# Kernel tuning notes

Hardware: AMD Instinct MI355X
Metric: run time of the kernel (lower is better)

The kernel has to match this reference:

```python
import jax, jax.numpy as jnp
import numpy as np

B, F, T, C, G = 2, 2048, 750, 20, 3
K = int(T * 0.125)  # top-k for score_pre


def _conv1d(x, w, b=None, pad=0):
    # x: (N, Cin, L), w: (Cout, Cin, k)
    out = jax.lax.conv_general_dilated(x, w, (1,), [(pad, pad)],
                                       dimension_numbers=('NCH', 'OIH', 'NCH'))
    return out if b is None else out + b[None, :, None]


def _base(x, w1, b1, w2, b2):
    # BaseModule: two k=3 convs with LeakyReLU(0.01); dropout = identity (eval)
    h = jax.nn.leaky_relu(_conv1d(x, w1, b1, pad=1))
    h = jax.nn.leaky_relu(_conv1d(h, w2, b2, pad=1))
    return h


def _post_cls(feat_agg, w1, b1, w2, b2, wc, batch, g):
    # feat_agg: (batch*C, F, g) -> BaseModule -> grouped 1x1 classifier -> mean over g
    h = _base(feat_agg, w1, b1, w2, b2)            # (batch*C, 2048, g)
    h = h.reshape(batch, C, 2048, g)
    score = jnp.einsum('bckg,ck->bcg', h, wc[:, :, 0])  # grouped conv1d, groups=C
    return score.mean(axis=2)                       # (batch, C)


def setup_inputs():
    key = jax.random.key(0)
    ks = jax.random.split(key, 8)
    s = 0.02
    x = jax.random.normal(ks[0], (B, F, T), jnp.float32)
    w1 = jax.random.normal(ks[1], (2048, F, 3), jnp.float32) * s
    b1 = jnp.zeros((2048,), jnp.float32)
    w2 = jax.random.normal(ks[2], (2048, 2048, 3), jnp.float32) * s
    b2 = jnp.zeros((2048,), jnp.float32)
    wc = jax.random.normal(ks[3], (C, 2048, 1), jnp.float32) * s   # classifier, no bias
    watt = jax.random.normal(ks[4], (C, C, 1), jnp.float32) * s    # attention 1x1 conv
    batt = jnp.zeros((C,), jnp.float32)
    cls_label = (jax.random.uniform(ks[5], (B, C)) < 0.15).astype(jnp.int32)
    cls_label = cls_label.at[:, 0].set(1)  # guarantee >=1 gt class per video
    return {'x': x, 'w1': w1, 'b1': b1, 'w2': w2, 'b2': b2, 'wc': wc,
            'watt': watt, 'batt': batt, 'cls_label': cls_label,
            'groups': G, 'is_train': 1}


def reference(x, w1, b1, w2, b2, wc, watt, batt, cls_label, groups, is_train):
    g = groups
    Tg = T // g
    seq_cas = _conv1d(_base(x, w1, b1, w2, b2), wc)           # (B, C, T)
    score_pre = jax.lax.top_k(seq_cas, K)[0].mean(axis=2)     # (B, C)
    wa = jax.nn.sigmoid(_conv1d(seq_cas, watt, batt))         # (B, C, T) attention weights

    # _agg_feature: strided slice t = j*g + i  <=>  reshape T -> (Tg, g), group idx last
    xg = x.reshape(B, F, Tg, g)
    wag = wa.reshape(B, C, Tg, g)
    feat_agg = jnp.einsum('bcjg,bfjg->bcfg', wag, xg).reshape(B * C, F, g)
    score_post = _post_cls(feat_agg, w1, b1, w2, b2, wc, B, g)  # (B, C)

    if is_train:
        # background stream, vectorized over (batch, suppressed class c) with masking
        wbg = (1.0 - wa).reshape(B, C, Tg, g)
        # tiny intermediate (B,C,C,Tg,g), then contract with features
        ww = jnp.einsum('bajg,bcjg->bcajg', wag, wbg)
        agg = jnp.einsum('bcajg,bfjg->bcafg', ww, xg).reshape(B * C * C, F, g)
        sc = _post_cls(agg, w1, b1, w2, b2, wc, B * C, g).reshape(B, C, C)  # [b, suppressed c, class a]
        m = cls_label.astype(score_post.dtype)                 # (B, C) multi-hot
        ngt = jnp.maximum(m.sum(axis=1, keepdims=True), 1.0)
        collect = jnp.einsum('bc,bca->ba', m, sc) / ngt        # mean over gt classes
        diag = jnp.diagonal(sc, axis1=1, axis2=2)              # sc[b, j, j]
        collect = jnp.where(m > 0, diag, collect)              # overwrite gt entries
        score_agg = jax.nn.softmax(jnp.concatenate([score_post, collect], axis=1), axis=1)
        return (score_pre, score_post, score_agg)
    else:
        return (jax.nn.softmax(score_pre, axis=1), seq_cas)
```

## Files before the change

kernel.cpp:

```cpp
#include <hip/hip_runtime.h>
#include <math.h>

namespace {
constexpr int kF = 2048;
constexpr int kT = 750;
constexpr int kC = 20;
constexpr int kTop = 93;
}

typedef __bf16 bf16x8 __attribute__((ext_vector_type(8)));
typedef float f32x4 __attribute__((ext_vector_type(4)));

__device__ __forceinline__ ushort f2bf(float f) {
  uint u = __builtin_bit_cast(uint, f);
  uint r = u + 0x7FFFu + ((u >> 16) & 1u);
  return (ushort)(r >> 16);
}
__device__ __forceinline__ float bf2f(ushort u) {
  return __builtin_bit_cast(float, ((uint)u) << 16);
}
__device__ __forceinline__ float leaky(float v) { return v > 0.f ? v : 0.01f * v; }

__device__ __forceinline__ void gload_lds16(const ushort* g, ushort* l) {
  __builtin_amdgcn_global_load_lds(
      (const __attribute__((address_space(1))) void*)g,
      (__attribute__((address_space(3))) void*)l, 16, 0, 0);
}

__global__ void build_list_kernel(const int* __restrict__ lbl,
                                  int4* __restrict__ meta, int* __restrict__ cnt) {
  if (threadIdx.x != 0) return;
  int n = 0;
  for (int b = 0; b < 2; ++b) {
    cnt[4 + b] = n;
    for (int c = 0; c < kC; ++c) { meta[n] = make_int4(b, c, c, 1); ++n; }
    for (int c = 0; c < kC; ++c)
      for (int a = 0; a < kC; ++a)
        if (lbl[b * kC + c] > 0 || c == a) { meta[n] = make_int4(b, c, a, 0); ++n; }
    cnt[6 + b] = (n - cnt[4 + b]);
  }
  cnt[0] = n;
  cnt[1] = n * 3;
  cnt[2] = 1500;
  cnt[3] = 0;
}

__global__ __launch_bounds__(256) void convert_w_kernel(
    const float* __restrict__ w1, const float* __restrict__ w2,
    ushort* __restrict__ Wt1, ushort* __restrict__ Wt2,
    ushort* __restrict__ zpage) {
  const int co = blockIdx.x;
  const float* w = (blockIdx.y == 0) ? w1 : w2;
  ushort* Wt = (blockIdx.y == 0) ? Wt1 : Wt2;
  const int ci0 = threadIdx.x * 8;
  float v[24];
  const float4* p = (const float4*)(w + (size_t)co * 6144 + ci0 * 3);
#pragma unroll
  for (int s = 0; s < 6; ++s) {
    float4 f = p[s];
    v[s * 4 + 0] = f.x; v[s * 4 + 1] = f.y; v[s * 4 + 2] = f.z; v[s * 4 + 3] = f.w;
  }
#pragma unroll
  for (int tap = 0; tap < 3; ++tap) {
    ushort o[8];
#pragma unroll
    for (int j = 0; j < 8; ++j) o[j] = f2bf(v[j * 3 + tap]);
    ushort4 a = {o[0], o[1], o[2], o[3]}, b = {o[4], o[5], o[6], o[7]};
    ushort4* q = (ushort4*)(Wt + (size_t)tap * kF * kF + (size_t)co * kF + ci0);
    q[0] = a; q[1] = b;
  }
  if (blockIdx.x == 0 && blockIdx.y == 0) {
    ((float4*)zpage)[threadIdx.x] = (float4){0.f, 0.f, 0.f, 0.f};
  }
}

__global__ __launch_bounds__(256) void convert_kernel(
    const float* __restrict__ src, ushort* __restrict__ dst, int n) {
  int i = (blockIdx.x * 256 + threadIdx.x) * 4;
  if (i + 3 < n) {
    float4 f = *(const float4*)(src + i);
    ushort4 o;
    o.x = f2bf(f.x); o.y = f2bf(f.y); o.z = f2bf(f.z); o.w = f2bf(f.w);
    *(ushort4*)(dst + i) = o;
  } else {
    for (; i < n; ++i) dst[i] = f2bf(src[i]);
  }
}

__global__ __launch_bounds__(256) void transpose_kernel(
    const float* __restrict__ x, ushort* __restrict__ xTt) {
  __shared__ float tile[64][65];
  const int b = blockIdx.z;
  const int t0 = blockIdx.x * 64, f0 = blockIdx.y * 64;
  const int tx = threadIdx.x & 63, ty4 = threadIdx.x >> 6;
#pragma unroll
  for (int i = 0; i < 16; ++i) {
    int lf = ty4 + i * 4;
    int t = t0 + tx;
    tile[lf][tx] = (t < kT) ? x[((size_t)b * kF + f0 + lf) * kT + t] : 0.f;
  }
  __syncthreads();
#pragma unroll
  for (int i = 0; i < 16; ++i) {
    int lt = ty4 + i * 4;
    int t = t0 + lt;
    if (t < kT)
      xTt[(size_t)(b * kT + t) * kF + f0 + tx] = f2bf(tile[tx][lt]);
  }
}

__global__ __launch_bounds__(256) void xj_kernel(
    const float* __restrict__ x, ushort* __restrict__ xJ) {
  const int bid = blockIdx.x;
  const int b = bid >> 11, f = bid & 2047;
  __shared__ float buf[768];
  const float* xr = x + ((size_t)b * kF + f) * kT;
  for (int t = threadIdx.x; t < kT; t += 256) buf[t] = xr[t];
  __syncthreads();
  const int j = threadIdx.x;
#pragma unroll
  for (int g = 0; g < 3; ++g) {
    float v = (j < 250) ? buf[j * 3 + g] : 0.f;
    xJ[(((size_t)(b * 3 + g) * kF + f) << 8) + j] = f2bf(v);
  }
}

__global__ __launch_bounds__(256) void ww_build_kernel(
    const float* __restrict__ wab, const int4* __restrict__ meta,
    const int* __restrict__ cnt, ushort* __restrict__ W2) {
  const int bg = blockIdx.x;
  const int b = bg / 3, g = bg % 3;
  const int r0 = blockIdx.y * 32;
  const int nb = cnt[6 + b], boff = cnt[4 + b];
  if (r0 >= nb) return;
  __shared__ float ws[kC][256];
  for (int i = threadIdx.x; i < kC * 250; i += 256) {
    int c = i / 250, j = i % 250;
    ws[c][j] = wab[(size_t)(b * kC + c) * kT + j * 3 + g];
  }
  __syncthreads();
  ushort* Wb = W2 + (size_t)bg * 512 * 256;
  const int j = threadIdx.x;
  for (int rr = 0; rr < 32; ++rr) {
    int r = r0 + rr;
    if (r >= nb) break;
    int4 m = meta[boff + r];
    float v = 0.f;
    if (j < 250)
      v = m.w ? ws[m.y][j] : ws[m.z][j] * (1.f - ws[m.y][j]);
    Wb[(size_t)r * 256 + j] = f2bf(v);
  }
}

__global__ __launch_bounds__(256) void ww_gemm_kernel(
    const ushort* __restrict__ xJ, const ushort* __restrict__ W2,
    const int* __restrict__ cnt, ushort* __restrict__ FeatY) {
  const int bg = blockIdx.z;
  const int b = bg / 3, g = bg % 3;
  const int nb = cnt[6 + b], boff = cnt[4 + b];
  const int s0 = blockIdx.x * 128;
  if (s0 >= nb) return;
  __shared__ ushort sA[2][128 * 64];
  __shared__ ushort sB[2][128 * 64];
  const int tid = threadIdx.x;
  const int w = tid >> 6, lane = tid & 63;
  const int wm = w >> 1, wn = w & 1;
  const int f0 = blockIdx.y * 128;
  const ushort* A = xJ + ((size_t)bg * kF << 8);
  const ushort* Bp = W2 + (size_t)bg * 512 * 256;
  const int srow = lane >> 3;
  const int selem = ((lane & 7) ^ srow) * 8;
  f32x4 acc[4][4];
#pragma unroll
  for (int i = 0; i < 4; ++i)
#pragma unroll
    for (int j = 0; j < 4; ++j) acc[i][j] = (f32x4){0.f, 0.f, 0.f, 0.f};

  auto STAGE = [&](int buf, int kt) {
    const int kin = kt * 64;
#pragma unroll
    for (int i = 0; i < 4; ++i) {
      int r = (w * 4 + i) * 8 + srow;
      gload_lds16(A + (size_t)(f0 + r) * 256 + kin + selem,
                  &sA[buf][(w * 4 + i) * 512]);
    }
#pragma unroll
    for (int i = 0; i < 4; ++i) {
      int r = (w * 4 + i) * 8 + srow;
      gload_lds16(Bp + (size_t)(s0 + r) * 256 + kin + selem,
                  &sB[buf][(w * 4 + i) * 512]);
    }
  };

  STAGE(0, 0);
  asm volatile("s_waitcnt vmcnt(0)" ::: "memory");
  __builtin_amdgcn_s_barrier();

  int cur = 0;
  for (int kt = 0; kt < 4; ++kt) {
    if (kt + 1 < 4) STAGE(cur ^ 1, kt + 1);
#pragma unroll
    for (int ksub = 0; ksub < 2; ++ksub) {
      bf16x8 af[4], bfv[4];
      const int rlow = lane & 7;
#pragma unroll
      for (int fm = 0; fm < 4; ++fm) {
        int row = wm * 64 + fm * 16 + (lane & 15);
        int c16 = (ksub * 4 + (lane >> 4)) ^ rlow;
        af[fm] = *(const bf16x8*)&sA[cur][row * 64 + c16 * 8];
      }
#pragma unroll
      for (int fn = 0; fn < 4; ++fn) {
        int row = wn * 64 + fn * 16 + (lane & 15);
        int c16 = (ksub * 4 + (lane >> 4)) ^ rlow;
        bfv[fn] = *(const bf16x8*)&sB[cur][row * 64 + c16 * 8];
      }
#pragma unroll
      for (int fm = 0; fm < 4; ++fm)
#pragma unroll
        for (int fn = 0; fn < 4; ++fn)
          acc[fm][fn] = __builtin_amdgcn_mfma_f32_16x16x32_bf16(
              af[fm], bfv[fn], acc[fm][fn], 0, 0, 0);
    }
    asm volatile("s_waitcnt vmcnt(0)" ::: "memory");
    __builtin_amdgcn_s_barrier();
    cur ^= 1;
  }

#pragma unroll
  for (int fm = 0; fm < 4; ++fm) {
#pragma unroll
    for (int fn = 0; fn < 4; ++fn) {
      int s = s0 + wn * 64 + fn * 16 + (lane & 15);
      if (s >= nb) continue;
      int row = f0 + wm * 64 + fm * 16 + ((lane >> 4) << 2);
      ushort4 o;
      o.x = f2bf(acc[fm][fn][0]);
      o.y = f2bf(acc[fm][fn][1]);
      o.z = f2bf(acc[fm][fn][2]);
      o.w = f2bf(acc[fm][fn][3]);
      *(ushort4*)&FeatY[(size_t)((boff + s) * 3 + g) * kF + row] = o;
    }
  }
}

template <int L>
__global__ __launch_bounds__(512, 1) void gemm_conv_kernel(
    const ushort* __restrict__ A, const ushort* __restrict__ B,
    const ushort* __restrict__ zpage, ushort* __restrict__ Cpart,
    const int* __restrict__ ncp, int NP, int ktn_base, int ktrem) {
  extern __shared__ ushort lds[];
  const int nc = *ncp;
  const int tid = threadIdx.x;
  const int wid = tid >> 6, lane = tid & 63;
  const int wr = wid >> 2, wc = wid & 3;
  const int gx = gridDim.x, gy = gridDim.y;
  const int nwg = gx * gy * gridDim.z;
  const int h = blockIdx.x + gx * (blockIdx.y + gy * blockIdx.z);
  const int lgc = (h & 7) * (nwg >> 3) + (h >> 3);
  const int bx = lgc % gx;
  const int byz = lgc / gx;
  const int co0 = (byz % gy) * 256;
  const int col0 = bx * 256;
  if (col0 >= nc) return;
  const int z = byz / gy;
  const int kt0 = z * ktn_base + (z < ktrem ? z : ktrem);
  const int ktn = ktn_base + (z < ktrem ? 1 : 0);
  const int ktend = kt0 + ktn;

  const int pofs = lane >> 3;
  const int lin_s = (lane & 7) ^ pofs;
  const int mofs = 2 * pofs + (lin_s >> 2);
  const int qseg = (lin_s & 3) * 8;
  const int l15 = lane & 15;
  const int seg8 = ((((l15 & 1) << 2) + (lane >> 4)) ^ (l15 >> 1)) * 8;
  const int off_rl = (l15 >> 1) * 64 + seg8;

  f32x4 acc[8][4];
#pragma unroll
  for (int i = 0; i < 8; ++i)
#pragma unroll
    for (int j = 0; j < 4; ++j) acc[i][j] = (f32x4){0.f, 0.f, 0.f, 0.f};

  auto STAGE_A = [&](int buf, int kt) {
    const int tap = kt >> 6;
    const int kin = (kt & 63) * 32;
    const size_t abase = (size_t)tap * kF * kF + kin + qseg;
#pragma unroll
    for (int l = 0; l < 2; ++l) {
      int m = l * 128 + wid * 16 + mofs;
      gload_lds16(A + abase + (size_t)(co0 + m) * kF,
                  &lds[buf * 16384 + l * 4096 + wid * 512]);
    }
  };
  auto STAGE_B = [&](int buf, int kt) {
    const int tap = kt >> 6;
    const int kin = (kt & 63) * 32;
#pragma unroll
    for (int l = 0; l < 2; ++l) {
      int m = l * 128 + wid * 16 + mofs;
      int col = col0 + m;
      int t = col - (col / L) * L;
      int tt = t + tap - 1;
      const ushort* src = (col < nc && tt >= 0 && tt < L)
          ? B + (size_t)(col + tap - 1) * kF + kin + qseg
          : zpage + qseg;
      gload_lds16(src, &lds[buf * 16384 + 8192 + l * 4096 + wid * 512]);
    }
  };

  STAGE_A(kt0 & 3, kt0);           STAGE_B(kt0 & 3, kt0);
  STAGE_A((kt0 + 1) & 3, kt0 + 1); STAGE_B((kt0 + 1) & 3, kt0 + 1);
  STAGE_A((kt0 + 2) & 3, kt0 + 2); STAGE_B((kt0 + 2) & 3, kt0 + 2);
  asm volatile("s_waitcnt vmcnt(8)" ::: "memory");
  __builtin_amdgcn_s_barrier();
  __builtin_amdgcn_sched_barrier(0);

  for (int kt = kt0; kt < ktend; ++kt) {
    const int buf = kt & 3;
    const int ts = (kt + 3 < ktend) ? kt + 3 : ktend - 1;
    const int bufs = ts & 3;
    const ushort* bb = &lds[buf * 16384];
    STAGE_A(bufs, ts);
    STAGE_B(bufs, ts);
    bf16x8 bfv[4], af[8];
#pragma unroll
    for (int fn = 0; fn < 4; ++fn)
      bfv[fn] = *(const bf16x8*)&bb[8192 + wc * 2048 + fn * 512 + off_rl];
#pragma unroll
    for (int fm = 0; fm < 8; ++fm)
      af[fm] = *(const bf16x8*)&bb[wr * 4096 + fm * 512 + off_rl];
    __builtin_amdgcn_s_setprio(1);
#pragma unroll
    for (int fm = 0; fm < 8; ++fm)
#pragma unroll
      for (int fn = 0; fn < 4; ++fn)
        acc[fm][fn] = __builtin_amdgcn_mfma_f32_16x16x32_bf16(
            af[fm], bfv[fn], acc[fm][fn], 0, 0, 0);
    __builtin_amdgcn_s_setprio(0);
    asm volatile("s_waitcnt vmcnt(8)" ::: "memory");
    __builtin_amdgcn_s_barrier();
    __builtin_amdgcn_sched_barrier(0);
  }

  ushort* Cz = Cpart + (size_t)z * NP * kF;
#pragma unroll
  for (int fm = 0; fm < 8; ++fm) {
#pragma unroll
    for (int fn = 0; fn < 4; ++fn) {
      int col = col0 + wc * 64 + fn * 16 + l15;
      int row = co0 + wr * 128 + fm * 16 + ((lane >> 4) << 2);
      ushort4 o;
      o.x = f2bf(acc[fm][fn][0]);
      o.y = f2bf(acc[fm][fn][1]);
      o.z = f2bf(acc[fm][fn][2]);
      o.w = f2bf(acc[fm][fn][3]);
      *(ushort4*)&Cz[(size_t)col * kF + row] = o;
    }
  }
}

__global__ __launch_bounds__(256) void reduce_kernel(
    const ushort* __restrict__ Cpart, const float* __restrict__ bias,
    ushort* __restrict__ Y, const int* __restrict__ ncp, int NP, int S) {
  const int col = blockIdx.x;
  if (col >= *ncp) return;
  const int row0 = threadIdx.x * 8;
  float s[8] = {};
  for (int z = 0; z < S; ++z) {
    const ushort* p = &Cpart[((size_t)z * NP + col) * kF + row0];
    ushort4 a = *(const ushort4*)p;
    ushort4 b = *(const ushort4*)(p + 4);
    s[0] += bf2f(a.x); s[1] += bf2f(a.y); s[2] += bf2f(a.z); s[3] += bf2f(a.w);
    s[4] += bf2f(b.x); s[5] += bf2f(b.y); s[6] += bf2f(b.z); s[7] += bf2f(b.w);
  }
  float4 bv0 = *(const float4*)&bias[row0];
  float4 bv1 = *(const float4*)&bias[row0 + 4];
  ushort4 o0, o1;
  o0.x = f2bf(leaky(s[0] + bv0.x)); o0.y = f2bf(leaky(s[1] + bv0.y));
  o0.z = f2bf(leaky(s[2] + bv0.z)); o0.w = f2bf(leaky(s[3] + bv0.w));
  o1.x = f2bf(leaky(s[4] + bv1.x)); o1.y = f2bf(leaky(s[5] + bv1.y));
  o1.z = f2bf(leaky(s[6] + bv1.z)); o1.w = f2bf(leaky(s[7] + bv1.w));
  *(ushort4*)&Y[(size_t)col * kF + row0] = o0;
  *(ushort4*)&Y[(size_t)col * kF + row0 + 4] = o1;
}

__global__ __launch_bounds__(256) void reduce_cls_kernel(
    const ushort* __restrict__ Cpart, const float* __restrict__ bias,
    const float* __restrict__ wc, const int4* __restrict__ meta,
    const int* __restrict__ cnt, float* __restrict__ scpart, int NP, int S) {
  __shared__ float red[256];
  const int col = blockIdx.x;
  if (col >= cnt[1]) return;
  const int4 m = meta[col / 3];
  const int cls = m.w ? m.y : m.z;
  const int row0 = threadIdx.x * 8;
  float s[8] = {};
  for (int z = 0; z < S; ++z) {
    const ushort* p = &Cpart[((size_t)z * NP + col) * kF + row0];
    ushort4 a = *(const ushort4*)p;
    ushort4 b = *(const ushort4*)(p + 4);
    s[0] += bf2f(a.x); s[1] += bf2f(a.y); s[2] += bf2f(a.z); s[3] += bf2f(a.w);
    s[4] += bf2f(b.x); s[5] += bf2f(b.y); s[6] += bf2f(b.z); s[7] += bf2f(b.w);
  }
  float4 bv0 = *(const float4*)&bias[row0];
  float4 bv1 = *(const float4*)&bias[row0 + 4];
  float4 w0 = *(const float4*)&wc[(size_t)cls * kF + row0];
  float4 w1 = *(const float4*)&wc[(size_t)cls * kF + row0 + 4];
  float acc =
      bf2f(f2bf(leaky(s[0] + bv0.x))) * w0.x + bf2f(f2bf(leaky(s[1] + bv0.y))) * w0.y +
      bf2f(f2bf(leaky(s[2] + bv0.z))) * w0.z + bf2f(f2bf(leaky(s[3] + bv0.w))) * w0.w +
      bf2f(f2bf(leaky(s[4] + bv1.x))) * w1.x + bf2f(f2bf(leaky(s[5] + bv1.y))) * w1.y +
      bf2f(f2bf(leaky(s[6] + bv1.z))) * w1.z + bf2f(f2bf(leaky(s[7] + bv1.w))) * w1.w;
  red[threadIdx.x] = acc;
  __syncthreads();
  for (int t = 128; t > 0; t >>= 1) {
    if (threadIdx.x < t) red[threadIdx.x] += red[threadIdx.x + t];
    __syncthreads();
  }
  if (threadIdx.x == 0) scpart[col] = red[0];
}

__global__ __launch_bounds__(256) void cls2_kernel(
    const float* __restrict__ scpart, const int4* __restrict__ meta,
    const int* __restrict__ cnt, float* __restrict__ out40,
    float* __restrict__ scb) {
  const int n = blockIdx.x * 256 + threadIdx.x;
  if (n >= cnt[0]) return;
  const int4 m = meta[n];
  float v = (scpart[3 * n] + scpart[3 * n + 1] + scpart[3 * n + 2]) * (1.f / 3.f);
  if (m.w) out40[m.x * kC + m.y] = v;
  else scb[m.x * 400 + m.y * kC + m.z] = v;
}

__global__ __launch_bounds__(256) void seqcas_kernel(
    const ushort* __restrict__ h2, const ushort* __restrict__ wcb,
    const float* __restrict__ watt, const float* __restrict__ batt,
    float* __restrict__ seq, float* __restrict__ wa) {
  const int w = threadIdx.x >> 6, lane = threadIdx.x & 63;
  const int idx = blockIdx.x * 4 + w;
  if (idx >= 2 * kT) return;
  const ushort* hr = h2 + (size_t)idx * kF;
  float acc[kC];
#pragma unroll
  for (int c = 0; c < kC; ++c) acc[c] = 0.f;
#pragma unroll
  for (int ch = 0; ch < 4; ++ch) {
    const int ci0 = ch * 512 + lane * 8;
    ushort4 ha = *(const ushort4*)(hr + ci0);
    ushort4 hb = *(const ushort4*)(hr + ci0 + 4);
    float hx[8] = {bf2f(ha.x), bf2f(ha.y), bf2f(ha.z), bf2f(ha.w),
                   bf2f(hb.x), bf2f(hb.y), bf2f(hb.z), bf2f(hb.w)};
#pragma unroll
    for (int c = 0; c < kC; ++c) {
      const ushort* wr = wcb + c * kF + ci0;
      ushort4 wa4 = *(const ushort4*)wr;
      ushort4 wb4 = *(const ushort4*)(wr + 4);
      acc[c] += bf2f(wa4.x) * hx[0] + bf2f(wa4.y) * hx[1] +
                bf2f(wa4.z) * hx[2] + bf2f(wa4.w) * hx[3] +
                bf2f(wb4.x) * hx[4] + bf2f(wb4.y) * hx[5] +
                bf2f(wb4.z) * hx[6] + bf2f(wb4.w) * hx[7];
    }
  }
#pragma unroll
  for (int off = 32; off; off >>= 1)
#pragma unroll
    for (int c = 0; c < kC; ++c) acc[c] += __shfl_xor(acc[c], off);
  if (lane == 0) {
    int b = idx / kT, t = idx % kT;
#pragma unroll
    for (int c = 0; c < kC; ++c) seq[(size_t)(b * kC + c) * kT + t] = acc[c];
#pragma unroll
    for (int c = 0; c < kC; ++c) {
      float z = batt[c];
#pragma unroll
      for (int a = 0; a < kC; ++a) z += watt[c * kC + a] * acc[a];
      wa[(size_t)(b * kC + c) * kT + t] = 1.f / (1.f + expf(-z));
    }
  }
}

__global__ __launch_bounds__(64) void score_pre_kernel(
    const float* __restrict__ seq, float* __restrict__ out) {
  const int n = blockIdx.x;
  const int lane = threadIdx.x;
  float v[12];
#pragma unroll
  for (int i = 0; i < 12; ++i) {
    int idx = lane + i * 64;
    v[i] = (idx < kT) ? seq[(size_t)n * kT + idx] : -1e30f;
  }
  float sum = 0.f;
  for (int it = 0; it < kTop; ++it) {
    float lm = v[0];
#pragma unroll
    for (int i = 1; i < 12; ++i) lm = fmaxf(lm, v[i]);
    float wm = lm;
#pragma unroll
    for (int off = 32; off; off >>= 1) wm = fmaxf(wm, __shfl_xor(wm, off));
    sum += wm;
    unsigned long long ball = __ballot(lm == wm);
    int first = __ffsll(ball) - 1;
    bool own = (lane == first);
    bool done = false;
#pragma unroll
    for (int i = 0; i < 12; ++i) {
      bool hit = own && !done && (v[i] == wm);
      if (hit) { v[i] = -1e30f; done = true; }
    }
  }
  if (lane == 0) out[n] = sum / (float)kTop;
}

__global__ void final_kernel(const float* __restrict__ score_post,
                             const float* __restrict__ sc_buf,
                             const int* __restrict__ label,
                             float* __restrict__ out) {
  __shared__ float z[2 * kC];
  __shared__ float collect[kC];
  const int b = blockIdx.x;
  const int tid = threadIdx.x;
  if (tid < kC) {
    int a = tid;
    float s = 0.f, ngt = 0.f;
    for (int c = 0; c < kC; ++c) {
      if (label[b * kC + c] > 0) {
        ngt += 1.f;
        s += sc_buf[b * 400 + c * kC + a];
      }
    }
    if (ngt < 1.f) ngt = 1.f;
    float col = s / ngt;
    if (label[b * kC + a] > 0) col = sc_buf[b * 400 + a * kC + a];
    collect[a] = col;
  }
  __syncthreads();
  if (tid < 2 * kC) z[tid] = (tid < kC) ? score_post[b * kC + tid] : collect[tid - kC];
  __syncthreads();
  if (tid == 0) {
    float mx = z[0];
    for (int i = 1; i < 2 * kC; ++i) mx = fmaxf(mx, z[i]);
    float s = 0.f;
    for (int i = 0; i < 2 * kC; ++i) { z[i] = expf(z[i] - mx); s += z[i]; }
    for (int i = 0; i < 2 * kC; ++i) out[80 + b * 2 * kC + i] = z[i] / s;
  }
}

extern "C" void kernel_launch(void* const* d_in, const int* in_sizes, int n_in,
                              void* d_out, int out_size, void* d_ws, size_t ws_size,
                              hipStream_t stream) {
  (void)in_sizes; (void)n_in; (void)out_size;
  const float* x    = (const float*)d_in[0];
  const float* w1   = (const float*)d_in[1];
  const float* b1   = (const float*)d_in[2];
  const float* w2   = (const float*)d_in[3];
  const float* b2   = (const float*)d_in[4];
  const float* wc   = (const float*)d_in[5];
  const float* watt = (const float*)d_in[6];
  const float* batt = (const float*)d_in[7];
  const int*   lbl  = (const int*)d_in[8];
  float* out = (float*)d_out;
  char*  wsb = (char*)d_ws;

  hipFuncSetAttribute(reinterpret_cast<const void*>(&gemm_conv_kernel<750>),
                      hipFuncAttributeMaxDynamicSharedMemorySize, 131072);
  hipFuncSetAttribute(reinterpret_cast<const void*>(&gemm_conv_kernel<3>),
                      hipFuncAttributeMaxDynamicSharedMemorySize, 131072);

  ushort* Wt1   = (ushort*)(wsb + 0);
  ushort* Wt2   = (ushort*)(wsb + 25165824);
  ushort* wcb   = (ushort*)(wsb + 50331648);
  ushort* zpage = (ushort*)(wsb + 50413568);
  ushort* xTt   = (ushort*)(wsb + 50417664);
  ushort* xJ    = (ushort*)(wsb + 56561664);
  ushort* W2b   = (ushort*)(wsb + 62853120);
  ushort* Ybuf  = (ushort*)(wsb + 64425984);
  ushort* h2    = (ushort*)(wsb + 74747904);
  float*  scpart= (float*)(wsb + 80891904);
  float*  seq   = (float*)(wsb + 91213824);
  float*  wab   = (float*)(wsb + 91333824);
  float*  scb   = (float*)(wsb + 91453824);
  int*    cnt   = (int*)(wsb + 91457024);
  int4*   meta  = (int4*)(wsb + 91457088);
  ushort* Ppart = (ushort*)(wsb + 91470848);

  const int S_main = 5;
  const size_t ppart_off = 91470848;
  const size_t avail = (ws_size > ppart_off) ? ws_size - ppart_off : 0;
  const int S_post = (avail >= (size_t)8 * 2560 * 2048 * 2) ? 8
                   : (avail >= (size_t)6 * 2560 * 2048 * 2) ? 6 : 4;
  const int ktn_post = 192 / S_post;

  dim3 blk(256);
  build_list_kernel<<<dim3(1), dim3(64), 0, stream>>>(lbl, meta, cnt);
  convert_w_kernel<<<dim3(2048, 2), blk, 0, stream>>>(w1, w2, Wt1, Wt2, zpage);
  convert_kernel<<<dim3(40), blk, 0, stream>>>(wc, wcb, kC * kF);
  transpose_kernel<<<dim3(12, 32, 2), blk, 0, stream>>>(x, xTt);
  xj_kernel<<<dim3(4096), blk, 0, stream>>>(x, xJ);
  gemm_conv_kernel<750><<<dim3(6, 8, S_main), dim3(512), 131072, stream>>>(
      Wt1, xTt, zpage, Ppart, &cnt[2], 1536, 38, 2);
  reduce_kernel<<<dim3(1500), blk, 0, stream>>>(Ppart, b1, Ybuf, &cnt[2], 1536, S_main);
  gemm_conv_kernel<750><<<dim3(6, 8, S_main), dim3(512), 131072, stream>>>(
      Wt2, Ybuf, zpage, Ppart, &cnt[2], 1536, 38, 2);
  reduce_kernel<<<dim3(1500), blk, 0, stream>>>(Ppart, b2, h2, &cnt[2], 1536, S_main);
  seqcas_kernel<<<dim3(375), blk, 0, stream>>>(h2, wcb, watt, batt, seq, wab);
  score_pre_kernel<<<dim3(40), dim3(64), 0, stream>>>(seq, out);
  ww_build_kernel<<<dim3(6, 16), blk, 0, stream>>>(wab, meta, cnt, W2b);
  ww_gemm_kernel<<<dim3(4, 16, 6), blk, 0, stream>>>(xJ, W2b, cnt, Ybuf);
  gemm_conv_kernel<3><<<dim3(10, 8, S_post), dim3(512), 131072, stream>>>(
      Wt1, Ybuf, zpage, Ppart, &cnt[1], 2560, ktn_post, 0);
  reduce_kernel<<<dim3(2520), blk, 0, stream>>>(Ppart, b1, Ybuf, &cnt[1], 2560, S_post);
  gemm_conv_kernel<3><<<dim3(10, 8, S_post), dim3(512), 131072, stream>>>(
      Wt2, Ybuf, zpage, Ppart, &cnt[1], 2560, ktn_post, 0);
  reduce_cls_kernel<<<dim3(2520), blk, 0, stream>>>(
      Ppart, b2, wc, meta, cnt, scpart, 2560, S_post);
  cls2_kernel<<<dim3(4), blk, 0, stream>>>(scpart, meta, cnt, out + 40, scb);
  final_kernel<<<dim3(2), dim3(64), 0, stream>>>(out + 40, scb, lbl, out);
}
```

Measured before the change: 358.0 us.

## Merge prep kernels, fuse reduce with seqcas, and split GEMM MFMA loop in halves

The preparation kernels (list build, weight and wc conversion, transpose, xJ) are folded into two launches, which cuts launch overhead. The second-conv reduce is fused with the seq_cas and attention computation, so the bf16 h2 round-trip through memory is no longer needed. The GEMM inner loop now loads half of the A fragments, runs 16 MFMAs, issues the B stage, then loads and computes the second half. This is meant to lower register pressure and interleave the global-to-LDS copies with compute. The added lgkmcnt waits could serialize the LDS reads, and the fused reduce keeps bf16 rounding of the partial sums but drops the bf16 rounding of h2.

```diff
diff --git a/kernel.cpp b/kernel.cpp
--- a/kernel.cpp
+++ b/kernel.cpp
@@ -27,28 +27,12 @@
       (__attribute__((address_space(3))) void*)l, 16, 0, 0);
 }
 
-__global__ void build_list_kernel(const int* __restrict__ lbl,
-                                  int4* __restrict__ meta, int* __restrict__ cnt) {
-  if (threadIdx.x != 0) return;
-  int n = 0;
-  for (int b = 0; b < 2; ++b) {
-    cnt[4 + b] = n;
-    for (int c = 0; c < kC; ++c) { meta[n] = make_int4(b, c, c, 1); ++n; }
-    for (int c = 0; c < kC; ++c)
-      for (int a = 0; a < kC; ++a)
-        if (lbl[b * kC + c] > 0 || c == a) { meta[n] = make_int4(b, c, a, 0); ++n; }
-    cnt[6 + b] = (n - cnt[4 + b]);
-  }
-  cnt[0] = n;
-  cnt[1] = n * 3;
-  cnt[2] = 1500;
-  cnt[3] = 0;
-}
-
-__global__ __launch_bounds__(256) void convert_w_kernel(
+__global__ __launch_bounds__(256) void prep_w_kernel(
     const float* __restrict__ w1, const float* __restrict__ w2,
+    const float* __restrict__ wc, const int* __restrict__ lbl,
     ushort* __restrict__ Wt1, ushort* __restrict__ Wt2,
-    ushort* __restrict__ zpage) {
+    ushort* __restrict__ wcb, ushort* __restrict__ zpage,
+    int4* __restrict__ meta, int* __restrict__ cnt) {
   const int co = blockIdx.x;
   const float* w = (blockIdx.y == 0) ? w1 : w2;
   ushort* Wt = (blockIdx.y == 0) ? Wt1 : Wt2;
@@ -69,59 +53,64 @@
     ushort4* q = (ushort4*)(Wt + (size_t)tap * kF * kF + (size_t)co * kF + ci0);
     q[0] = a; q[1] = b;
   }
+  if (blockIdx.y == 0 && co < 160) {
+    int i = co * 256 + threadIdx.x;
+    wcb[i] = f2bf(wc[i]);
+  }
   if (blockIdx.x == 0 && blockIdx.y == 0) {
     ((float4*)zpage)[threadIdx.x] = (float4){0.f, 0.f, 0.f, 0.f};
   }
-}
-
-__global__ __launch_bounds__(256) void convert_kernel(
-    const float* __restrict__ src, ushort* __restrict__ dst, int n) {
-  int i = (blockIdx.x * 256 + threadIdx.x) * 4;
-  if (i + 3 < n) {
-    float4 f = *(const float4*)(src + i);
-    ushort4 o;
-    o.x = f2bf(f.x); o.y = f2bf(f.y); o.z = f2bf(f.z); o.w = f2bf(f.w);
-    *(ushort4*)(dst + i) = o;
+  if (blockIdx.x == 0 && blockIdx.y == 1 && threadIdx.x == 0) {
+    int n = 0;
+    for (int b = 0; b < 2; ++b) {
+      cnt[4 + b] = n;
+      for (int c = 0; c < kC; ++c) { meta[n] = make_int4(b, c, c, 1); ++n; }
+      for (int c = 0; c < kC; ++c)
+        for (int a = 0; a < kC; ++a)
+          if (lbl[b * kC + c] > 0 || c == a) { meta[n] = make_int4(b, c, a, 0); ++n; }
+      cnt[6 + b] = (n - cnt[4 + b]);
+    }
+    cnt[0] = n; cnt[1] = n * 3; cnt[2] = 1500; cnt[3] = 0;
+  }
+}
+
+__global__ __launch_bounds__(256) void prep_x_kernel(
+    const float* __restrict__ x, ushort* __restrict__ xTt,
+    ushort* __restrict__ xJ) {
+  __shared__ float tile[64][65];
+  __shared__ float buf[768];
+  const int blk = blockIdx.x;
+  if (blk < 768) {
+    const int b = blk / 384, r = blk % 384;
+    const int by = r / 12, bx = r % 12;
+    const int t0 = bx * 64, f0 = by * 64;
+    const int tx = threadIdx.x & 63, ty4 = threadIdx.x >> 6;
+#pragma unroll
+    for (int i = 0; i < 16; ++i) {
+      int lf = ty4 + i * 4;
+      int t = t0 + tx;
+      tile[lf][tx] = (t < kT) ? x[((size_t)b * kF + f0 + lf) * kT + t] : 0.f;
+    }
+    __syncthreads();
+#pragma unroll
+    for (int i = 0; i < 16; ++i) {
+      int lt = ty4 + i * 4;
+      int t = t0 + lt;
+      if (t < kT)
+        xTt[(size_t)(b * kT + t) * kF + f0 + tx] = f2bf(tile[tx][lt]);
+    }
   } else {
-    for (; i < n; ++i) dst[i] = f2bf(src[i]);
-  }
-}
-
-__global__ __launch_bounds__(256) void transpose_kernel(
-    const float* __restrict__ x, ushort* __restrict__ xTt) {
-  __shared__ float tile[64][65];
-  const int b = blockIdx.z;
-  const int t0 = blockIdx.x * 64, f0 = blockIdx.y * 64;
-  const int tx = threadIdx.x & 63, ty4 = threadIdx.x >> 6;
-#pragma unroll
-  for (int i = 0; i < 16; ++i) {
-    int lf = ty4 + i * 4;
-    int t = t0 + tx;
-    tile[lf][tx] = (t < kT) ? x[((size_t)b * kF + f0 + lf) * kT + t] : 0.f;
-  }
-  __syncthreads();
-#pragma unroll
-  for (int i = 0; i < 16; ++i) {
-    int lt = ty4 + i * 4;
-    int t = t0 + lt;
-    if (t < kT)
-      xTt[(size_t)(b * kT + t) * kF + f0 + tx] = f2bf(tile[tx][lt]);
-  }
-}
-
-__global__ __launch_bounds__(256) void xj_kernel(
-    const float* __restrict__ x, ushort* __restrict__ xJ) {
-  const int bid = blockIdx.x;
-  const int b = bid >> 11, f = bid & 2047;
-  __shared__ float buf[768];
-  const float* xr = x + ((size_t)b * kF + f) * kT;
-  for (int t = threadIdx.x; t < kT; t += 256) buf[t] = xr[t];
-  __syncthreads();
-  const int j = threadIdx.x;
-#pragma unroll
-  for (int g = 0; g < 3; ++g) {
-    float v = (j < 250) ? buf[j * 3 + g] : 0.f;
-    xJ[(((size_t)(b * 3 + g) * kF + f) << 8) + j] = f2bf(v);
+    const int bid = blk - 768;
+    const int b = bid >> 11, f = bid & 2047;
+    const float* xr = x + ((size_t)b * kF + f) * kT;
+    for (int t = threadIdx.x; t < kT; t += 256) buf[t] = xr[t];
+    __syncthreads();
+    const int j = threadIdx.x;
+#pragma unroll
+    for (int g = 0; g < 3; ++g) {
+      float v = (j < 250) ? buf[j * 3 + g] : 0.f;
+      xJ[(((size_t)(b * 3 + g) * kF + f) << 8) + j] = f2bf(v);
+    }
   }
 }
 
@@ -321,22 +310,37 @@
     const int ts = (kt + 3 < ktend) ? kt + 3 : ktend - 1;
     const int bufs = ts & 3;
     const ushort* bb = &lds[buf * 16384];
+    bf16x8 bfv[4], af[4];
     STAGE_A(bufs, ts);
-    STAGE_B(bufs, ts);
-    bf16x8 bfv[4], af[8];
 #pragma unroll
     for (int fn = 0; fn < 4; ++fn)
       bfv[fn] = *(const bf16x8*)&bb[8192 + wc * 2048 + fn * 512 + off_rl];
 #pragma unroll
-    for (int fm = 0; fm < 8; ++fm)
+    for (int fm = 0; fm < 4; ++fm)
       af[fm] = *(const bf16x8*)&bb[wr * 4096 + fm * 512 + off_rl];
+    asm volatile("s_waitcnt lgkmcnt(0)" ::: "memory");
+    __builtin_amdgcn_sched_barrier(0);
     __builtin_amdgcn_s_setprio(1);
 #pragma unroll
-    for (int fm = 0; fm < 8; ++fm)
+    for (int fm = 0; fm < 4; ++fm)
 #pragma unroll
       for (int fn = 0; fn < 4; ++fn)
         acc[fm][fn] = __builtin_amdgcn_mfma_f32_16x16x32_bf16(
             af[fm], bfv[fn], acc[fm][fn], 0, 0, 0);
+    __builtin_amdgcn_s_setprio(0);
+    STAGE_B(bufs, ts);
+#pragma unroll
+    for (int fm = 0; fm < 4; ++fm)
+      af[fm] = *(const bf16x8*)&bb[wr * 4096 + (fm + 4) * 512 + off_rl];
+    asm volatile("s_waitcnt lgkmcnt(0)" ::: "memory");
+    __builtin_amdgcn_sched_barrier(0);
+    __builtin_amdgcn_s_setprio(1);
+#pragma unroll
+    for (int fm = 0; fm < 4; ++fm)
+#pragma unroll
+      for (int fn = 0; fn < 4; ++fn)
+        acc[fm + 4][fn] = __builtin_amdgcn_mfma_f32_16x16x32_bf16(
+            af[fm], bfv[fn], acc[fm + 4][fn], 0, 0, 0);
     __builtin_amdgcn_s_setprio(0);
     asm volatile("s_waitcnt vmcnt(8)" ::: "memory");
     __builtin_amdgcn_s_barrier();
@@ -383,6 +387,64 @@
   o1.z = f2bf(leaky(s[6] + bv1.z)); o1.w = f2bf(leaky(s[7] + bv1.w));
   *(ushort4*)&Y[(size_t)col * kF + row0] = o0;
   *(ushort4*)&Y[(size_t)col * kF + row0 + 4] = o1;
+}
+
+__global__ __launch_bounds__(256) void reduce_seqcas_kernel(
+    const ushort* __restrict__ Cpart, const float* __restrict__ bias,
+    const ushort* __restrict__ wcb, const float* __restrict__ watt,
+    const float* __restrict__ batt, float* __restrict__ seq,
+    float* __restrict__ wa, int NP, int S) {
+  __shared__ float red[4][kC];
+  __shared__ float sseq[kC];
+  const int col = blockIdx.x;
+  const int tid = threadIdx.x;
+  const int wid = tid >> 6, lane = tid & 63;
+  const int row0 = tid * 8;
+  float s[8] = {};
+  for (int z = 0; z < S; ++z) {
+    const ushort* p = &Cpart[((size_t)z * NP + col) * kF + row0];
+    ushort4 a4 = *(const ushort4*)p;
+    ushort4 b4 = *(const ushort4*)(p + 4);
+    s[0] += bf2f(a4.x); s[1] += bf2f(a4.y); s[2] += bf2f(a4.z); s[3] += bf2f(a4.w);
+    s[4] += bf2f(b4.x); s[5] += bf2f(b4.y); s[6] += bf2f(b4.z); s[7] += bf2f(b4.w);
+  }
+  float4 bv0 = *(const float4*)&bias[row0];
+  float4 bv1 = *(const float4*)&bias[row0 + 4];
+  float a[8];
+  a[0] = leaky(s[0] + bv0.x); a[1] = leaky(s[1] + bv0.y);
+  a[2] = leaky(s[2] + bv0.z); a[3] = leaky(s[3] + bv0.w);
+  a[4] = leaky(s[4] + bv1.x); a[5] = leaky(s[5] + bv1.y);
+  a[6] = leaky(s[6] + bv1.z); a[7] = leaky(s[7] + bv1.w);
+  float p[kC];
+#pragma unroll
+  for (int c = 0; c < kC; ++c) {
+    const ushort* wr = wcb + (size_t)c * kF + row0;
+    ushort4 wa4 = *(const ushort4*)wr;
+    ushort4 wb4 = *(const ushort4*)(wr + 4);
+    p[c] = bf2f(wa4.x) * a[0] + bf2f(wa4.y) * a[1] +
+           bf2f(wa4.z) * a[2] + bf2f(wa4.w) * a[3] +
+           bf2f(wb4.x) * a[4] + bf2f(wb4.y) * a[5] +
+           bf2f(wb4.z) * a[6] + bf2f(wb4.w) * a[7];
+  }
+#pragma unroll
+  for (int off = 32; off; off >>= 1)
+#pragma unroll
+    for (int c = 0; c < kC; ++c) p[c] += __shfl_xor(p[c], off);
+  if (lane == 0)
+#pragma unroll
+    for (int c = 0; c < kC; ++c) red[wid][c] = p[c];
+  __syncthreads();
+  if (tid < kC)
+    sseq[tid] = red[0][tid] + red[1][tid] + red[2][tid] + red[3][tid];
+  __syncthreads();
+  if (tid < kC) {
+    float z = batt[tid];
+#pragma unroll
+    for (int a2 = 0; a2 < kC; ++a2) z += watt[tid * kC + a2] * sseq[a2];
+    const int b = col / kT, t = col - b * kT;
+    seq[(size_t)(b * kC + tid) * kT + t] = sseq[tid];
+    wa[(size_t)(b * kC + tid) * kT + t] = 1.f / (1.f + expf(-z));
+  }
 }
 
 __global__ __launch_bounds__(256) void reduce_cls_kernel(
@@ -433,53 +495,6 @@
   else scb[m.x * 400 + m.y * kC + m.z] = v;
 }
 
-__global__ __launch_bounds__(256) void seqcas_kernel(
-    const ushort* __restrict__ h2, const ushort* __restrict__ wcb,
-    const float* __restrict__ watt, const float* __restrict__ batt,
-    float* __restrict__ seq, float* __restrict__ wa) {
-  const int w = threadIdx.x >> 6, lane = threadIdx.x & 63;
-  const int idx = blockIdx.x * 4 + w;
-  if (idx >= 2 * kT) return;
-  const ushort* hr = h2 + (size_t)idx * kF;
-  float acc[kC];
-#pragma unroll
-  for (int c = 0; c < kC; ++c) acc[c] = 0.f;
-#pragma unroll
-  for (int ch = 0; ch < 4; ++ch) {
-    const int ci0 = ch * 512 + lane * 8;
-    ushort4 ha = *(const ushort4*)(hr + ci0);
-    ushort4 hb = *(const ushort4*)(hr + ci0 + 4);
-    float hx[8] = {bf2f(ha.x), bf2f(ha.y), bf2f(ha.z), bf2f(ha.w),
-                   bf2f(hb.x), bf2f(hb.y), bf2f(hb.z), bf2f(hb.w)};
-#pragma unroll
-    for (int c = 0; c < kC; ++c) {
-      const ushort* wr = wcb + c * kF + ci0;
-      ushort4 wa4 = *(const ushort4*)wr;
-      ushort4 wb4 = *(const ushort4*)(wr + 4);
-      acc[c] += bf2f(wa4.x) * hx[0] + bf2f(wa4.y) * hx[1] +
-                bf2f(wa4.z) * hx[2] + bf2f(wa4.w) * hx[3] +
-                bf2f(wb4.x) * hx[4] + bf2f(wb4.y) * hx[5] +
-                bf2f(wb4.z) * hx[6] + bf2f(wb4.w) * hx[7];
-    }
-  }
-#pragma unroll
-  for (int off = 32; off; off >>= 1)
-#pragma unroll
-    for (int c = 0; c < kC; ++c) acc[c] += __shfl_xor(acc[c], off);
-  if (lane == 0) {
-    int b = idx / kT, t = idx % kT;
-#pragma unroll
-    for (int c = 0; c < kC; ++c) seq[(size_t)(b * kC + c) * kT + t] = acc[c];
-#pragma unroll
-    for (int c = 0; c < kC; ++c) {
-      float z = batt[c];
-#pragma unroll
-      for (int a = 0; a < kC; ++a) z += watt[c * kC + a] * acc[a];
-      wa[(size_t)(b * kC + c) * kT + t] = 1.f / (1.f + expf(-z));
-    }
-  }
-}
-
 __global__ __launch_bounds__(64) void score_pre_kernel(
     const float* __restrict__ seq, float* __restrict__ out) {
   const int n = blockIdx.x;
@@ -575,8 +590,7 @@
   ushort* xJ    = (ushort*)(wsb + 56561664);
   ushort* W2b   = (ushort*)(wsb + 62853120);
   ushort* Ybuf  = (ushort*)(wsb + 64425984);
-  ushort* h2    = (ushort*)(wsb + 74747904);
-  float*  scpart= (float*)(wsb + 80891904);
+  float*  scpart= (float*)(wsb + 74747904);
   float*  seq   = (float*)(wsb + 91213824);
   float*  wab   = (float*)(wsb + 91333824);
   float*  scb   = (float*)(wsb + 91453824);
@@ -592,18 +606,16 @@
   const int ktn_post = 192 / S_post;
 
   dim3 blk(256);
-  build_list_kernel<<<dim3(1), dim3(64), 0, stream>>>(lbl, meta, cnt);
-  convert_w_kernel<<<dim3(2048, 2), blk, 0, stream>>>(w1, w2, Wt1, Wt2, zpage);
-  convert_kernel<<<dim3(40), blk, 0, stream>>>(wc, wcb, kC * kF);
-  transpose_kernel<<<dim3(12, 32, 2), blk, 0, stream>>>(x, xTt);
-  xj_kernel<<<dim3(4096), blk, 0, stream>>>(x, xJ);
+  prep_w_kernel<<<dim3(2048, 2), blk, 0, stream>>>(
+      w1, w2, wc, lbl, Wt1, Wt2, wcb, zpage, meta, cnt);
+  prep_x_kernel<<<dim3(4864), blk, 0, stream>>>(x, xTt, xJ);
   gemm_conv_kernel<750><<<dim3(6, 8, S_main), dim3(512), 131072, stream>>>(
       Wt1, xTt, zpage, Ppart, &cnt[2], 1536, 38, 2);
   reduce_kernel<<<dim3(1500), blk, 0, stream>>>(Ppart, b1, Ybuf, &cnt[2], 1536, S_main);
   gemm_conv_kernel<750><<<dim3(6, 8, S_main), dim3(512), 131072, stream>>>(
       Wt2, Ybuf, zpage, Ppart, &cnt[2], 1536, 38, 2);
-  reduce_kernel<<<dim3(1500), blk, 0, stream>>>(Ppart, b2, h2, &cnt[2], 1536, S_main);
-  seqcas_kernel<<<dim3(375), blk, 0, stream>>>(h2, wcb, watt, batt, seq, wab);
+  reduce_seqcas_kernel<<<dim3(1500), blk, 0, stream>>>(
+      Ppart, b2, wcb, watt, batt, seq, wab, 1536, S_main);
   score_pre_kernel<<<dim3(40), dim3(64), 0, stream>>>(seq, out);
   ww_build_kernel<<<dim3(6, 16), blk, 0, stream>>>(wab, meta, cnt, W2b);
   ww_gemm_kernel<<<dim3(4, 16, 6), blk, 0, stream>>>(xJ, W2b, cnt, Ybuf);
```

After: 311.1 us. 1.15x faster.
